# Optimization experiments

Measured on AMD Instinct MI355X. Metric: run time of the kernel, lower is better.

Reference implementation:

```python
import jax, jax.numpy as jnp
import numpy as np

N, E, G = 50000, 800000, 128
F_IN, F0, D, NL, DN = 128, 256, 256, 4, 512


def setup_inputs() -> dict:
    key = jax.random.key(0)
    ks = iter(jax.random.split(key, 40))

    def U(shape, fan_in):
        s = 1.0 / np.sqrt(fan_in)
        return jax.random.uniform(next(ks), shape, minval=-s, maxval=s, dtype=jnp.float32)

    x = jax.random.normal(next(ks), (N, F_IN), dtype=jnp.float32)
    edge_index = jax.random.randint(next(ks), (2, E), 0, N)
    batch_index = jnp.sort(jax.random.randint(next(ks), (N,), 0, G))
    return dict(
        x=x, edge_index=edge_index, batch_index=batch_index,
        fl_W=U((F_IN, F0), F_IN), fl_b=U((F0,), F_IN),
        conv1_W=U((F0, D), F0), conv1_b=U((D,), F0),
        tr1_W=U((D, D), D), tr1_b=U((D,), D),
        bn1_g=jnp.ones((D,), jnp.float32), bn1_b=jnp.zeros((D,), jnp.float32),
        convs_W=U((NL, D, D), D), convs_b=U((NL, D), D),
        trs_W=U((NL, D, D), D), trs_b=U((NL, D), D),
        bns_g=jnp.ones((NL, D), jnp.float32), bns_b=jnp.zeros((NL, D), jnp.float32),
        l1_W=U((2 * D, DN), 2 * D), l1_b=U((DN,), 2 * D),
        l2_W=U((DN, DN // 2), DN), l2_b=U((DN // 2,), DN),
        l3_W=U((DN // 2, 10), DN // 2), l3_b=U((10,), DN // 2),
    )


def reference(x, edge_index, batch_index, fl_W, fl_b, conv1_W, conv1_b,
              tr1_W, tr1_b, bn1_g, bn1_b, convs_W, convs_b, trs_W, trs_b,
              bns_g, bns_b, l1_W, l1_b, l2_W, l2_b, l3_W, l3_b):
    n = x.shape[0]
    loops = jnp.arange(n, dtype=edge_index.dtype)
    src = jnp.concatenate([edge_index[0], loops])  # [E+N] GCN self-loops
    dst = jnp.concatenate([edge_index[1], loops])
    deg = jax.ops.segment_sum(jnp.ones_like(dst, dtype=x.dtype), dst, num_segments=n)
    dis = jax.lax.rsqrt(deg)  # deg >= 1 due to self-loops
    norm = dis[src] * dis[dst]  # [E+N] symmetric normalization

    def gcn(h, W, b):
        m = h @ W
        return jax.ops.segment_sum(norm[:, None] * m[src], dst, num_segments=n) + b

    def bn(h, g, bb):
        mu = h.mean(axis=0)
        var = jnp.mean((h - mu) ** 2, axis=0)  # biased var, torch BN train math
        return g * (h - mu) * jax.lax.rsqrt(var + 1e-5) + bb

    h = x @ fl_W + fl_b
    h = jax.nn.relu(gcn(h, conv1_W, conv1_b))
    h = bn(h, bn1_g, bn1_b)
    h = jax.nn.relu(h @ tr1_W + tr1_b)  # dropout off (eval)
    for i in range(convs_W.shape[0]):
        h = jax.nn.relu(gcn(h, convs_W[i], convs_b[i]))
        h = bn(h, bns_g[i], bns_b[i])
        h = jax.nn.relu(h @ trs_W[i] + trs_b[i])

    sums = jax.ops.segment_sum(h, batch_index, num_segments=G)
    cnt = jax.ops.segment_sum(jnp.ones((n,), h.dtype), batch_index, num_segments=G)
    pooled = sums / jnp.maximum(cnt, 1.0)[:, None]  # global_mean_pool
    z = jnp.concatenate([pooled, pooled], axis=1)
    z = jax.nn.relu(z @ l1_W + l1_b)
    z = jax.nn.relu(z @ l2_W + l2_b)
    return z @ l3_W + l3_b
```

## Files before the change

### kernel.cpp

```cpp
#include <hip/hip_runtime.h>

#define DD 256

typedef unsigned short u16;
typedef unsigned int u32;
using bf16x8 = __attribute__((ext_vector_type(8))) short;
using f16x8  = __attribute__((ext_vector_type(8))) _Float16;
using f32x4  = __attribute__((ext_vector_type(4))) float;

#define GLB_PTR(p) ((const __attribute__((address_space(1))) u32*)(p))
#define LDS_PTR(p) ((__attribute__((address_space(3))) u32*)(p))


__device__ __forceinline__ u32 f2bfx2(float v) {
  u32 b = __float_as_uint(v);
  u32 hi = (b + 0x7fffu + ((b >> 16) & 1u)) >> 16;
  float hf = __uint_as_float(hi << 16);
  float lof = v - hf;
  u32 b2 = __float_as_uint(lof);
  u32 lo = (b2 + 0x7fffu + ((b2 >> 16) & 1u)) >> 16;
  return hi | (lo << 16);
}

__device__ __forceinline__ float bfx2_to_f(u32 e) {
  return __uint_as_float(e << 16) + __uint_as_float(e & 0xffff0000u);
}

__device__ __forceinline__ u16 f2h(float f) {
  _Float16 h = (_Float16)f;
  return __builtin_bit_cast(unsigned short, h);
}
__device__ __forceinline__ float h2f(u16 x) {
  return (float)__builtin_bit_cast(_Float16, x);
}

__device__ __forceinline__ bf16x8 as_bf16x8(uint4 u) {
  union { uint4 u; bf16x8 v; } c;
  c.u = u;
  return c.v;
}
__device__ __forceinline__ f16x8 as_f16x8(uint4 u) {
  union { uint4 u; f16x8 v; } c;
  c.u = u;
  return c.v;
}

__device__ __forceinline__ void unpack8(uint4 a, uint4 b, bf16x8& hi, bf16x8& lo) {
  union { u32 w[4]; bf16x8 v; } H, L;
  H.w[0] = __builtin_amdgcn_perm(a.y, a.x, 0x05040100u);
  L.w[0] = __builtin_amdgcn_perm(a.y, a.x, 0x07060302u);
  H.w[1] = __builtin_amdgcn_perm(a.w, a.z, 0x05040100u);
  L.w[1] = __builtin_amdgcn_perm(a.w, a.z, 0x07060302u);
  H.w[2] = __builtin_amdgcn_perm(b.y, b.x, 0x05040100u);
  L.w[2] = __builtin_amdgcn_perm(b.y, b.x, 0x07060302u);
  H.w[3] = __builtin_amdgcn_perm(b.w, b.z, 0x05040100u);
  L.w[3] = __builtin_amdgcn_perm(b.w, b.z, 0x07060302u);
  hi = H.v;
  lo = L.v;
}

__device__ __forceinline__ int packoff(int col, int k) {
  int w = col >> 6, r = (col >> 4) & 3, c16 = col & 15;
  int kc = k >> 5, q = (k >> 3) & 3, j = k & 7;
  return ((kc * 4 + w) * 4 + r) * 512 + (q * 16 + c16) * 8 + j;
}


__global__ void zero_i32_kernel(int* p, int n) {
  int i = blockIdx.x * 256 + threadIdx.x;
  if (i < n) p[i] = 0;
}

__global__ void zero_f32_kernel(float* p, int n) {
  int i = blockIdx.x * 256 + threadIdx.x;
  if (i < n) p[i] = 0.f;
}

__global__ void count_kernel(const int* __restrict__ dst, int* __restrict__ cnt, int e) {
  int i = blockIdx.x * 256 + threadIdx.x;
  if (i < e) atomicAdd(&cnt[dst[i]], 1);
}

__global__ void scan_block_kernel(const int* __restrict__ cnt, int* __restrict__ out,
                                  int* __restrict__ bsum, int n) {
  __shared__ int sh[256];
  int tid = threadIdx.x;
  int base = blockIdx.x * 1024 + tid * 4;
  int v0 = (base + 0 < n) ? cnt[base + 0] : 0;
  int v1 = (base + 1 < n) ? cnt[base + 1] : 0;
  int v2 = (base + 2 < n) ? cnt[base + 2] : 0;
  int v3 = (base + 3 < n) ? cnt[base + 3] : 0;
  int s = v0 + v1 + v2 + v3;
  sh[tid] = s;
  __syncthreads();
  for (int d = 1; d < 256; d <<= 1) {
    int t = (tid >= d) ? sh[tid - d] : 0;
    __syncthreads();
    sh[tid] += t;
    __syncthreads();
  }
  int excl = sh[tid] - s;
  if (base + 0 < n) out[base + 0] = excl;
  excl += v0;
  if (base + 1 < n) out[base + 1] = excl;
  excl += v1;
  if (base + 2 < n) out[base + 2] = excl;
  excl += v2;
  if (base + 3 < n) out[base + 3] = excl;
  if (tid == 255) bsum[blockIdx.x] = sh[255];
}

__global__ void scan_partials_kernel(int* bsum, int nb) {
  if (threadIdx.x == 0 && blockIdx.x == 0) {
    int acc = 0;
    for (int i = 0; i < nb; ++i) { int t = bsum[i]; bsum[i] = acc; acc += t; }
  }
}

__global__ void finalize_kernel(int* __restrict__ off, const int* __restrict__ bsum,
                                int* __restrict__ cursor, const int* __restrict__ cnt,
                                float* __restrict__ dis, int n, int e) {
  int i = blockIdx.x * 256 + threadIdx.x;
  if (i < n) {
    int o = off[i] + bsum[i >> 10];
    off[i] = o;
    cursor[i] = o;
    dis[i] = rsqrtf((float)(cnt[i] + 1));
  }
  if (i == 0 && blockIdx.x == 0) off[n] = e;
}

__global__ void fill_kernel(const int* __restrict__ src, const int* __restrict__ dst,
                            int* __restrict__ cursor, int* __restrict__ csr_src, int e) {
  int i = blockIdx.x * 256 + threadIdx.x;
  if (i < e) {
    int d = dst[i];
    int p = atomicAdd(&cursor[d], 1);
    csr_src[p] = src[i];
  }
}


__global__ void xsplit_kernel(const float* __restrict__ x, u32* __restrict__ xq, int n) {
  int i = blockIdx.x * 256 + threadIdx.x;
  if (i < n) xq[i] = f2bfx2(x[i]);
}


__global__ void wsplit_all_kernel(const float* __restrict__ fl_W, const float* __restrict__ conv1_W,
                                  const float* __restrict__ convs_W, u16* __restrict__ flHi,
                                  u16* __restrict__ flLo, u16* __restrict__ cvF) {
  int j = blockIdx.x;
  int m = blockIdx.y;
  int k = threadIdx.x;
  if (m == 0) {
    if (k < 128) {
      u32 p = f2bfx2(fl_W[(size_t)k * 256 + j]);
      int off = packoff(j, k);
      flHi[off] = (u16)(p & 0xffffu);
      flLo[off] = (u16)(p >> 16);
    }
  } else {
    int c = m - 1;
    const float* W = (c == 0) ? conv1_W : convs_W + (size_t)(c - 1) * 65536;
    cvF[(size_t)c * 65536 + packoff(j, k)] = f2h(W[(size_t)k * 256 + j]);
  }
}

__global__ void wsplit_fold_kernel(const float* __restrict__ W, const float* __restrict__ scale,
                                   const float* __restrict__ shift, const float* __restrict__ bt,
                                   u16* __restrict__ WhiT, u16* __restrict__ WloT,
                                   float* __restrict__ bias_out) {
  __shared__ float red[256];
  int j = blockIdx.x;
  int k = threadIdx.x;
  float w = W[(size_t)k * 256 + j];
  u32 p = f2bfx2(w * scale[k]);
  int off = packoff(j, k);
  WhiT[off] = (u16)(p & 0xffffu);
  WloT[off] = (u16)(p >> 16);
  red[k] = shift[k] * w;
  __syncthreads();
  for (int d = 128; d > 0; d >>= 1) {
    if (k < d) red[k] += red[k + d];
    __syncthreads();
  }
  if (k == 0) bias_out[j] = bt[j] + red[0];
}


__device__ __forceinline__ void afrag(const u32* Asbase, int R, int q, bf16x8& ah, bf16x8& al) {
  int s = (R & 7) << 4;
  const u32* row = Asbase + R * 32;
  uint4 a0 = *(const uint4*)(row + ((((q * 32)) ^ s) >> 2));
  uint4 a1 = *(const uint4*)(row + ((((q * 32) + 16) ^ s) >> 2));
  unpack8(a0, a1, ah, al);
}

template <int K, bool RELU>
__global__ __launch_bounds__(256) void gemm_mfma_kernel(
    const u32* __restrict__ Aq, const u16* __restrict__ WhiT, const u16* __restrict__ WloT,
    const float* __restrict__ bias, u16* __restrict__ Cv, int nrows) {
  constexpr int NK64 = K / 64;
  __shared__ __align__(16) u32 As[2][4096];
  const int tid = threadIdx.x;
  const int lane = tid & 63;
  const int wave = tid >> 6;
  const int row0 = blockIdx.x * 64;
  const int q = lane >> 4;
  const int r16 = lane & 15;

  int sRowG[4], sOff[4];
#pragma unroll
  for (int c = 0; c < 4; ++c) {
    int row_l = (c & 1) * 32 + wave * 8 + (lane >> 3);
    int grow = row0 + row_l;
    if (grow > nrows - 1) grow = nrows - 1;
    sRowG[c] = grow;
    sOff[c] = ((lane & 7) * 4) ^ ((row_l & 7) << 2);
  }

  int bBase[4];
#pragma unroll
  for (int r = 0; r < 4; ++r) bBase[r] = (wave * 4 + r) * 512 + lane * 8;

  f32x4 acc[4][4];
#pragma unroll
  for (int i = 0; i < 4; ++i)
#pragma unroll
    for (int r = 0; r < 4; ++r) acc[i][r] = (f32x4){0.f, 0.f, 0.f, 0.f};

  auto stage = [&](int buf, int kc64) {
#pragma unroll
    for (int c = 0; c < 4; ++c) {
      int chunk = c >> 1;
      const u32* gsrc = Aq + (size_t)sRowG[c] * K + kc64 * 64 + chunk * 32 + sOff[c];
      u32* ldst = &As[buf][chunk * 2048 + (c & 1) * 1024 + wave * 256];
      __builtin_amdgcn_global_load_lds(GLB_PTR(gsrc), LDS_PTR(ldst), 16, 0, 0);
    }
  };

  stage(0, 0);
  __syncthreads();

  int buf = 0;
#pragma unroll
  for (int kc = 0; kc < NK64; ++kc) {
    if (kc + 1 < NK64) stage(buf ^ 1, kc + 1);
#pragma unroll
    for (int ch = 0; ch < 2; ++ch) {
      const int kc32 = kc * 2 + ch;
      uint4 BH[4], BL[4];
#pragma unroll
      for (int r = 0; r < 4; ++r) {
        BH[r] = *(const uint4*)(WhiT + bBase[r] + kc32 * 8192);
        BL[r] = *(const uint4*)(WloT + bBase[r] + kc32 * 8192);
      }
      bf16x8 ah[4], al[4];
#pragma unroll
      for (int i = 0; i < 4; ++i) afrag(&As[buf][ch * 2048], i * 16 + r16, q, ah[i], al[i]);
#pragma unroll
      for (int r = 0; r < 4; ++r) {
        bf16x8 bh = as_bf16x8(BH[r]);
        bf16x8 bl = as_bf16x8(BL[r]);
#pragma unroll
        for (int i = 0; i < 4; ++i) {
          acc[i][r] = __builtin_amdgcn_mfma_f32_16x16x32_bf16(ah[i], bh, acc[i][r], 0, 0, 0);
          acc[i][r] = __builtin_amdgcn_mfma_f32_16x16x32_bf16(al[i], bh, acc[i][r], 0, 0, 0);
          acc[i][r] = __builtin_amdgcn_mfma_f32_16x16x32_bf16(ah[i], bl, acc[i][r], 0, 0, 0);
        }
      }
    }
    __syncthreads();
    buf ^= 1;
  }

#pragma unroll
  for (int r = 0; r < 4; ++r) {
    int col = wave * 64 + r * 16 + r16;
    float bv = bias ? bias[col] : 0.f;
#pragma unroll
    for (int i = 0; i < 4; ++i) {
#pragma unroll
      for (int g = 0; g < 4; ++g) {
        int row = row0 + i * 16 + q * 4 + g;
        if (row < nrows) {
          float v = acc[i][r][g] + bv;
          if (RELU) v = fmaxf(v, 0.f);
          Cv[(size_t)row * 256 + col] = f2h(v);
        }
      }
    }
  }
}

template <int K1, bool RELU1>
__global__ __launch_bounds__(256) void fused_gemm_kernel(
    const u32* __restrict__ Aq, const u16* __restrict__ W1h, const u16* __restrict__ W1l,
    const float* __restrict__ bias1, const u16* __restrict__ W2f, u16* __restrict__ C,
    int nrows) {
  constexpr int NK1 = K1 / 32;
  __shared__ __align__(16) u32 As[2][2048];
  __shared__ __align__(16) u16 T[64 * 256];
  const int tid = threadIdx.x;
  const int lane = tid & 63;
  const int wave = tid >> 6;
  const int row0 = blockIdx.x * 64;
  const int q = lane >> 4;
  const int r16 = lane & 15;

  int sRowG[2], sOff[2];
#pragma unroll
  for (int c = 0; c < 2; ++c) {
    int row_l = c * 32 + wave * 8 + (lane >> 3);
    int grow = row0 + row_l;
    if (grow > nrows - 1) grow = nrows - 1;
    sRowG[c] = grow;
    sOff[c] = ((lane & 7) * 4) ^ ((row_l & 7) << 2);
  }

  int bBase[4];
#pragma unroll
  for (int r = 0; r < 4; ++r) bBase[r] = (wave * 4 + r) * 512 + lane * 8;

  f32x4 acc[4][4];
#pragma unroll
  for (int i = 0; i < 4; ++i)
#pragma unroll
    for (int r = 0; r < 4; ++r) acc[i][r] = (f32x4){0.f, 0.f, 0.f, 0.f};

  auto stage = [&](int buf, int kc32) {
#pragma unroll
    for (int c = 0; c < 2; ++c) {
      const u32* gsrc = Aq + (size_t)sRowG[c] * K1 + kc32 * 32 + sOff[c];
      u32* ldst = &As[buf][c * 1024 + wave * 256];
      __builtin_amdgcn_global_load_lds(GLB_PTR(gsrc), LDS_PTR(ldst), 16, 0, 0);
    }
  };

  stage(0, 0);
  __syncthreads();
  int buf = 0;
#pragma unroll
  for (int kc = 0; kc < NK1; ++kc) {
    if (kc + 1 < NK1) stage(buf ^ 1, kc + 1);
    uint4 BH[4], BL[4];
#pragma unroll
    for (int r = 0; r < 4; ++r) {
      BH[r] = *(const uint4*)(W1h + bBase[r] + kc * 8192);
      BL[r] = *(const uint4*)(W1l + bBase[r] + kc * 8192);
    }
    bf16x8 ah[4], al[4];
#pragma unroll
    for (int i = 0; i < 4; ++i) afrag(As[buf], i * 16 + r16, q, ah[i], al[i]);
#pragma unroll
    for (int r = 0; r < 4; ++r) {
      bf16x8 bh = as_bf16x8(BH[r]);
      bf16x8 bl = as_bf16x8(BL[r]);
#pragma unroll
      for (int i = 0; i < 4; ++i) {
        acc[i][r] = __builtin_amdgcn_mfma_f32_16x16x32_bf16(ah[i], bh, acc[i][r], 0, 0, 0);
        acc[i][r] = __builtin_amdgcn_mfma_f32_16x16x32_bf16(al[i], bh, acc[i][r], 0, 0, 0);
        acc[i][r] = __builtin_amdgcn_mfma_f32_16x16x32_bf16(ah[i], bl, acc[i][r], 0, 0, 0);
      }
    }
    __syncthreads();
    buf ^= 1;
  }

#pragma unroll
  for (int r = 0; r < 4; ++r) {
    int col = wave * 64 + r * 16 + r16;
    float bv = bias1[col];
#pragma unroll
    for (int i = 0; i < 4; ++i) {
#pragma unroll
      for (int g = 0; g < 4; ++g) {
        int row = i * 16 + q * 4 + g;
        float v = acc[i][r][g] + bv;
        if (RELU1) v = fmaxf(v, 0.f);
        *(u16*)((char*)T + row * 512 + ((col * 2) ^ ((row & 7) << 4))) = f2h(v);
      }
    }
  }

#pragma unroll
  for (int i = 0; i < 4; ++i)
#pragma unroll
    for (int r = 0; r < 4; ++r) acc[i][r] = (f32x4){0.f, 0.f, 0.f, 0.f};

  __syncthreads();

#pragma unroll
  for (int kc = 0; kc < 8; ++kc) {
    uint4 BF[4];
#pragma unroll
    for (int r = 0; r < 4; ++r) BF[r] = *(const uint4*)(W2f + bBase[r] + kc * 8192);
    f16x8 af[4];
#pragma unroll
    for (int i = 0; i < 4; ++i) {
      int row = i * 16 + r16;
      int base = kc * 64 + q * 16;
      af[i] = as_f16x8(*(const uint4*)((char*)T + row * 512 + (base ^ ((row & 7) << 4))));
    }
#pragma unroll
    for (int r = 0; r < 4; ++r) {
      f16x8 bf = as_f16x8(BF[r]);
#pragma unroll
      for (int i = 0; i < 4; ++i)
        acc[i][r] = __builtin_amdgcn_mfma_f32_16x16x32_f16(af[i], bf, acc[i][r], 0, 0, 0);
    }
  }

#pragma unroll
  for (int r = 0; r < 4; ++r) {
    int col = wave * 64 + r * 16 + r16;
#pragma unroll
    for (int i = 0; i < 4; ++i) {
#pragma unroll
      for (int g = 0; g < 4; ++g) {
        int row = row0 + i * 16 + q * 4 + g;
        if (row < nrows) C[(size_t)row * 256 + col] = f2h(acc[i][r][g]);
      }
    }
  }
}


__global__ __launch_bounds__(256) void gather_kernel(
    const u16* __restrict__ m, const int* __restrict__ off,
    const int* __restrict__ csr_src, const float* __restrict__ dis,
    const float* __restrict__ bias, u32* __restrict__ out,
    float* __restrict__ shard, int n) {
  __shared__ float2 red[4][256];
  int wv = threadIdx.x >> 6;
  int lane = threadIdx.x & 63;
  int node = blockIdx.x * 4 + wv;
  float ax = 0.f, ay = 0.f, az = 0.f, aw = 0.f;
  if (node < n) {
    float di = dis[node];
    uint2 v = *(const uint2*)(m + (size_t)node * DD + lane * 4);
    float w = di * di;
    ax = w * h2f((u16)(v.x & 0xffff)); ay = w * h2f((u16)(v.x >> 16));
    az = w * h2f((u16)(v.y & 0xffff)); aw = w * h2f((u16)(v.y >> 16));
    int e0 = off[node], e1 = off[node + 1];
    int e = e0;
    for (; e + 3 < e1; e += 4) {
      int s0 = csr_src[e], s1 = csr_src[e + 1], s2 = csr_src[e + 2], s3 = csr_src[e + 3];
      float w0 = dis[s0] * di, w1 = dis[s1] * di, w2 = dis[s2] * di, w3 = dis[s3] * di;
      uint2 u0 = *(const uint2*)(m + (size_t)s0 * DD + lane * 4);
      uint2 u1 = *(const uint2*)(m + (size_t)s1 * DD + lane * 4);
      uint2 u2 = *(const uint2*)(m + (size_t)s2 * DD + lane * 4);
      uint2 u3 = *(const uint2*)(m + (size_t)s3 * DD + lane * 4);
      ax = fmaf(w0, h2f((u16)(u0.x & 0xffff)), ax); ay = fmaf(w0, h2f((u16)(u0.x >> 16)), ay);
      az = fmaf(w0, h2f((u16)(u0.y & 0xffff)), az); aw = fmaf(w0, h2f((u16)(u0.y >> 16)), aw);
      ax = fmaf(w1, h2f((u16)(u1.x & 0xffff)), ax); ay = fmaf(w1, h2f((u16)(u1.x >> 16)), ay);
      az = fmaf(w1, h2f((u16)(u1.y & 0xffff)), az); aw = fmaf(w1, h2f((u16)(u1.y >> 16)), aw);
      ax = fmaf(w2, h2f((u16)(u2.x & 0xffff)), ax); ay = fmaf(w2, h2f((u16)(u2.x >> 16)), ay);
      az = fmaf(w2, h2f((u16)(u2.y & 0xffff)), az); aw = fmaf(w2, h2f((u16)(u2.y >> 16)), aw);
      ax = fmaf(w3, h2f((u16)(u3.x & 0xffff)), ax); ay = fmaf(w3, h2f((u16)(u3.x >> 16)), ay);
      az = fmaf(w3, h2f((u16)(u3.y & 0xffff)), az); aw = fmaf(w3, h2f((u16)(u3.y >> 16)), aw);
    }
    for (; e < e1; ++e) {
      int s0 = csr_src[e];
      float w0 = dis[s0] * di;
      uint2 u0 = *(const uint2*)(m + (size_t)s0 * DD + lane * 4);
      ax = fmaf(w0, h2f((u16)(u0.x & 0xffff)), ax); ay = fmaf(w0, h2f((u16)(u0.x >> 16)), ay);
      az = fmaf(w0, h2f((u16)(u0.y & 0xffff)), az); aw = fmaf(w0, h2f((u16)(u0.y >> 16)), aw);
    }
    float4 bb = *(const float4*)(bias + lane * 4);
    ax = fmaxf(ax + bb.x, 0.f);
    ay = fmaxf(ay + bb.y, 0.f);
    az = fmaxf(az + bb.z, 0.f);
    aw = fmaxf(aw + bb.w, 0.f);
    uint4 oo;
    oo.x = f2bfx2(ax); oo.y = f2bfx2(ay); oo.z = f2bfx2(az); oo.w = f2bfx2(aw);
    *(uint4*)(out + (size_t)node * DD + lane * 4) = oo;
  }
  red[wv][lane * 4 + 0] = make_float2(ax, ax * ax);
  red[wv][lane * 4 + 1] = make_float2(ay, ay * ay);
  red[wv][lane * 4 + 2] = make_float2(az, az * az);
  red[wv][lane * 4 + 3] = make_float2(aw, aw * aw);
  __syncthreads();
  int c = threadIdx.x;
  float2 a = red[0][c], b2 = red[1][c], c2 = red[2][c], d2 = red[3][c];
  float s = (a.x + b2.x) + (c2.x + d2.x);
  float qq = (a.y + b2.y) + (c2.y + d2.y);
  float* sh = shard + (size_t)(blockIdx.x & 63) * 512;
  atomicAdd(&sh[c], s);
  atomicAdd(&sh[256 + c], qq);
}


__global__ void bn_finalize_kernel(const float* __restrict__ shard, const float* __restrict__ g,
                                   const float* __restrict__ b, float* __restrict__ scale,
                                   float* __restrict__ shift, float inv_n) {
  int c = threadIdx.x;
  float s = 0.f, q = 0.f;
  for (int i = 0; i < 64; ++i) {
    s += shard[(size_t)i * 512 + c];
    q += shard[(size_t)i * 512 + 256 + c];
  }
  float mu = s * inv_n;
  float var = q * inv_n - mu * mu;
  float inv = rsqrtf(var + 1e-5f);
  float sc = g[c] * inv;
  scale[c] = sc;
  shift[c] = b[c] - mu * sc;
}


__global__ void pool_kernel(const u16* __restrict__ h, const int* __restrict__ batch,
                            float* __restrict__ pooled, int n) {
  int g = blockIdx.x;
  int c = threadIdx.x;
  int lo = 0, hi = n;
  while (lo < hi) { int mid = (lo + hi) >> 1; if (batch[mid] < g) lo = mid + 1; else hi = mid; }
  int start = lo;
  hi = n;
  while (lo < hi) { int mid = (lo + hi) >> 1; if (batch[mid] <= g) lo = mid + 1; else hi = mid; }
  int end = lo;
  float a0 = 0.f, a1 = 0.f, a2 = 0.f, a3 = 0.f;
  int r = start;
  for (; r + 3 < end; r += 4) {
    a0 += h2f(h[(size_t)(r + 0) * DD + c]);
    a1 += h2f(h[(size_t)(r + 1) * DD + c]);
    a2 += h2f(h[(size_t)(r + 2) * DD + c]);
    a3 += h2f(h[(size_t)(r + 3) * DD + c]);
  }
  for (; r < end; ++r) a0 += h2f(h[(size_t)r * DD + c]);
  float s = (a0 + a1) + (a2 + a3);
  int cg = end - start;
  pooled[g * DD + c] = s / (float)(cg > 1 ? cg : 1);
}


__global__ void mlp1_kernel(const float* __restrict__ pooled, const float* __restrict__ W,
                            const float* __restrict__ b, float* __restrict__ out) {
  __shared__ float p[256];
  int g = blockIdx.x;
  int j = blockIdx.y * 256 + threadIdx.x;
  p[threadIdx.x] = pooled[g * 256 + threadIdx.x];
  __syncthreads();
  float acc = b[j];
#pragma unroll 8
  for (int k = 0; k < 512; ++k) acc = fmaf(p[k & 255], W[k * 512 + j], acc);
  out[g * 512 + j] = fmaxf(acc, 0.f);
}

__global__ void mlp2_kernel(const float* __restrict__ z1, const float* __restrict__ W,
                            const float* __restrict__ b, float* __restrict__ out) {
  __shared__ float p[512];
  int g = blockIdx.x;
  p[threadIdx.x] = z1[g * 512 + threadIdx.x];
  p[256 + threadIdx.x] = z1[g * 512 + 256 + threadIdx.x];
  __syncthreads();
  float acc = b[threadIdx.x];
#pragma unroll 8
  for (int k = 0; k < 512; ++k) acc = fmaf(p[k], W[k * 256 + threadIdx.x], acc);
  out[g * 256 + threadIdx.x] = fmaxf(acc, 0.f);
}

__global__ void mlp3_kernel(const float* __restrict__ z2, const float* __restrict__ W,
                            const float* __restrict__ b, float* __restrict__ out) {
  int g = blockIdx.x;
  int lane = threadIdx.x;
  float acc[10];
#pragma unroll
  for (int o = 0; o < 10; ++o) acc[o] = 0.f;
  for (int k = lane; k < 256; k += 64) {
    float v = z2[g * 256 + k];
#pragma unroll
    for (int o = 0; o < 10; ++o) acc[o] = fmaf(v, W[k * 10 + o], acc[o]);
  }
#pragma unroll
  for (int o = 0; o < 10; ++o) {
    float s = acc[o];
    for (int d = 32; d > 0; d >>= 1) s += __shfl_down(s, d);
    if (lane == 0) out[g * 10 + o] = s + b[o];
  }
}


extern "C" void kernel_launch(void* const* d_in, const int* in_sizes, int n_in,
                              void* d_out, int out_size, void* d_ws, size_t ws_size,
                              hipStream_t stream) {
  const float* x = (const float*)d_in[0];
  const int* ei = (const int*)d_in[1];
  const int* batch = (const int*)d_in[2];
  const float* fl_W = (const float*)d_in[3];
  const float* fl_b = (const float*)d_in[4];
  const float* conv1_W = (const float*)d_in[5];
  const float* conv1_b = (const float*)d_in[6];
  const float* tr1_W = (const float*)d_in[7];
  const float* tr1_b = (const float*)d_in[8];
  const float* bn1_g = (const float*)d_in[9];
  const float* bn1_b = (const float*)d_in[10];
  const float* convs_W = (const float*)d_in[11];
  const float* convs_b = (const float*)d_in[12];
  const float* trs_W = (const float*)d_in[13];
  const float* trs_b = (const float*)d_in[14];
  const float* bns_g = (const float*)d_in[15];
  const float* bns_b = (const float*)d_in[16];
  const float* l1_W = (const float*)d_in[17];
  const float* l1_b = (const float*)d_in[18];
  const float* l2_W = (const float*)d_in[19];
  const float* l2_b = (const float*)d_in[20];
  const float* l3_W = (const float*)d_in[21];
  const float* l3_b = (const float*)d_in[22];

  const int N = in_sizes[0] / 128;
  const int E = in_sizes[1] / 2;
  const int G = out_size / 10;
  const int NL = in_sizes[11] / (256 * 256);
  const int* src = ei;
  const int* dst = ei + E;

  char* ws = (char*)d_ws;
  size_t o = 0;
  auto alloc = [&](size_t bytes) -> char* {
    o = (o + 255) & ~(size_t)255;
    char* p = ws + o;
    o += bytes;
    return p;
  };
  u32* hA = (u32*)alloc((size_t)N * DD * 4);
  u16* mF = (u16*)alloc((size_t)N * DD * 2);
  u32* xq = (u32*)alloc((size_t)N * 128 * 4);
  float* dis = (float*)alloc((size_t)N * 4);
  int* cnt = (int*)alloc((size_t)N * 4);
  int* off = (int*)alloc((size_t)(N + 1) * 4);
  int* cursor = (int*)alloc((size_t)N * 4);
  int* bsum = (int*)alloc(64 * 4);
  int* csr = (int*)alloc((size_t)E * 4);
  float* shards = (float*)alloc((size_t)(1 + NL) * 64 * 512 * 4);
  float* scalev = (float*)alloc(256 * 4);
  float* shiftv = (float*)alloc(256 * 4);
  float* pooled = (float*)alloc((size_t)G * 256 * 4);
  float* z1 = (float*)alloc((size_t)G * 512 * 4);
  float* z2 = (float*)alloc((size_t)G * 256 * 4);
  u16* flHi = (u16*)alloc(128 * 256 * 2);
  u16* flLo = (u16*)alloc(128 * 256 * 2);
  u16* cvF = (u16*)alloc((size_t)(1 + NL) * 256 * 256 * 2);
  u16* trHi = (u16*)alloc(256 * 256 * 2);
  u16* trLo = (u16*)alloc(256 * 256 * 2);
  float* trBias = (float*)alloc(256 * 4);

  dim3 b256(256);
  const int nblk = (N + 63) / 64;

  zero_i32_kernel<<<(N + 255) / 256, b256, 0, stream>>>(cnt, N);
  count_kernel<<<(E + 255) / 256, b256, 0, stream>>>(dst, cnt, E);
  int nb = (N + 1023) / 1024;
  scan_block_kernel<<<nb, b256, 0, stream>>>(cnt, off, bsum, N);
  scan_partials_kernel<<<1, 64, 0, stream>>>(bsum, nb);
  finalize_kernel<<<(N + 255) / 256, b256, 0, stream>>>(off, bsum, cursor, cnt, dis, N, E);
  fill_kernel<<<(E + 255) / 256, b256, 0, stream>>>(src, dst, cursor, csr, E);

  xsplit_kernel<<<(N * 128 + 255) / 256, b256, 0, stream>>>(x, xq, N * 128);
  dim3 wgrid(256, 2 + NL);
  wsplit_all_kernel<<<wgrid, b256, 0, stream>>>(fl_W, conv1_W, convs_W, flHi, flLo, cvF);
  int shard_elems = (1 + NL) * 64 * 512;
  zero_f32_kernel<<<(shard_elems + 255) / 256, b256, 0, stream>>>(shards, shard_elems);

  fused_gemm_kernel<128, false><<<nblk, b256, 0, stream>>>(xq, flHi, flLo, fl_b, cvF, mF, N);

  for (int L = 0; L < 1 + NL; ++L) {
    const float* bc = (L == 0) ? conv1_b : convs_b + (size_t)(L - 1) * 256;
    const float* gg = (L == 0) ? bn1_g : bns_g + (size_t)(L - 1) * 256;
    const float* gb = (L == 0) ? bn1_b : bns_b + (size_t)(L - 1) * 256;
    const float* Wt = (L == 0) ? tr1_W : trs_W + (size_t)(L - 1) * 256 * 256;
    const float* bt = (L == 0) ? tr1_b : trs_b + (size_t)(L - 1) * 256;
    float* slot = shards + (size_t)L * 64 * 512;

    gather_kernel<<<(N + 3) / 4, b256, 0, stream>>>(mF, off, csr, dis, bc, hA, slot, N);
    bn_finalize_kernel<<<1, b256, 0, stream>>>(slot, gg, gb, scalev, shiftv, 1.0f / (float)N);
    wsplit_fold_kernel<<<256, b256, 0, stream>>>(Wt, scalev, shiftv, bt, trHi, trLo, trBias);
    if (L < NL) {
      fused_gemm_kernel<256, true><<<nblk, b256, 0, stream>>>(
          hA, trHi, trLo, trBias, cvF + (size_t)(L + 1) * 65536, mF, N);
    } else {
      gemm_mfma_kernel<256, true><<<nblk, b256, 0, stream>>>(hA, trHi, trLo, trBias, mF, N);
    }
  }

  pool_kernel<<<G, b256, 0, stream>>>(mF, batch, pooled, N);
  dim3 m1grid(G, 2);
  mlp1_kernel<<<m1grid, b256, 0, stream>>>(pooled, l1_W, l1_b, z1);
  mlp2_kernel<<<G, b256, 0, stream>>>(z1, l2_W, l2_b, z2);
  mlp3_kernel<<<G, 64, 0, stream>>>(z2, l3_W, l3_b, (float*)d_out);
}
```

Measured before the change: 806.3 us.

## Store hidden activations as fp16 and precompute edge weights in CSR

The post-aggregation activations drop from split-bf16 pairs (two values per element) to a single fp16 value. The transform GEMMs therefore run one f16 MFMA per tile instead of three bf16 MFMAs, and read half as many activation bytes. The CSR now stores (src, normalized weight) pairs, so the gather no longer does a dependent dis[src] lookup per edge. In exchange, the BN-folded transform and the activations lose precision, since they are now single fp16 instead of near-fp32 split bf16.

```diff
diff --git a/kernel.cpp b/kernel.cpp
--- a/kernel.cpp
+++ b/kernel.cpp
@@ -20,10 +20,6 @@
   u32 b2 = __float_as_uint(lof);
   u32 lo = (b2 + 0x7fffu + ((b2 >> 16) & 1u)) >> 16;
   return hi | (lo << 16);
-}
-
-__device__ __forceinline__ float bfx2_to_f(u32 e) {
-  return __uint_as_float(e << 16) + __uint_as_float(e & 0xffff0000u);
 }
 
 __device__ __forceinline__ u16 f2h(float f) {
@@ -131,12 +127,15 @@
 }
 
 __global__ void fill_kernel(const int* __restrict__ src, const int* __restrict__ dst,
-                            int* __restrict__ cursor, int* __restrict__ csr_src, int e) {
+                            int* __restrict__ cursor, const float* __restrict__ dis,
+                            int2* __restrict__ csrE, int e) {
   int i = blockIdx.x * 256 + threadIdx.x;
   if (i < e) {
+    int s = src[i];
     int d = dst[i];
     int p = atomicAdd(&cursor[d], 1);
-    csr_src[p] = src[i];
+    float w = dis[s] * dis[d];
+    csrE[p] = make_int2(s, __float_as_int(w));
   }
 }
 
@@ -169,16 +168,12 @@
 
 __global__ void wsplit_fold_kernel(const float* __restrict__ W, const float* __restrict__ scale,
                                    const float* __restrict__ shift, const float* __restrict__ bt,
-                                   u16* __restrict__ WhiT, u16* __restrict__ WloT,
-                                   float* __restrict__ bias_out) {
+                                   u16* __restrict__ trF, float* __restrict__ bias_out) {
   __shared__ float red[256];
   int j = blockIdx.x;
   int k = threadIdx.x;
   float w = W[(size_t)k * 256 + j];
-  u32 p = f2bfx2(w * scale[k]);
-  int off = packoff(j, k);
-  WhiT[off] = (u16)(p & 0xffffu);
-  WloT[off] = (u16)(p >> 16);
+  trF[packoff(j, k)] = f2h(w * scale[k]);
   red[k] = shift[k] * w;
   __syncthreads();
   for (int d = 128; d > 0; d >>= 1) {
@@ -189,7 +184,12 @@
 }
 
 
-__device__ __forceinline__ void afrag(const u32* Asbase, int R, int q, bf16x8& ah, bf16x8& al) {
+__device__ __forceinline__ f16x8 afrag16(const u32* As, int R, int q) {
+  int off = (q * 4) ^ (((R >> 1) & 3) << 2);
+  return as_f16x8(*(const uint4*)(As + R * 16 + off));
+}
+
+__device__ __forceinline__ void afrag32(const u32* Asbase, int R, int q, bf16x8& ah, bf16x8& al) {
   int s = (R & 7) << 4;
   const u32* row = Asbase + R * 32;
   uint4 a0 = *(const uint4*)(row + ((((q * 32)) ^ s) >> 2));
@@ -197,109 +197,11 @@
   unpack8(a0, a1, ah, al);
 }
 
-template <int K, bool RELU>
-__global__ __launch_bounds__(256) void gemm_mfma_kernel(
-    const u32* __restrict__ Aq, const u16* __restrict__ WhiT, const u16* __restrict__ WloT,
-    const float* __restrict__ bias, u16* __restrict__ Cv, int nrows) {
-  constexpr int NK64 = K / 64;
-  __shared__ __align__(16) u32 As[2][4096];
-  const int tid = threadIdx.x;
-  const int lane = tid & 63;
-  const int wave = tid >> 6;
-  const int row0 = blockIdx.x * 64;
-  const int q = lane >> 4;
-  const int r16 = lane & 15;
-
-  int sRowG[4], sOff[4];
-#pragma unroll
-  for (int c = 0; c < 4; ++c) {
-    int row_l = (c & 1) * 32 + wave * 8 + (lane >> 3);
-    int grow = row0 + row_l;
-    if (grow > nrows - 1) grow = nrows - 1;
-    sRowG[c] = grow;
-    sOff[c] = ((lane & 7) * 4) ^ ((row_l & 7) << 2);
-  }
-
-  int bBase[4];
-#pragma unroll
-  for (int r = 0; r < 4; ++r) bBase[r] = (wave * 4 + r) * 512 + lane * 8;
-
-  f32x4 acc[4][4];
-#pragma unroll
-  for (int i = 0; i < 4; ++i)
-#pragma unroll
-    for (int r = 0; r < 4; ++r) acc[i][r] = (f32x4){0.f, 0.f, 0.f, 0.f};
-
-  auto stage = [&](int buf, int kc64) {
-#pragma unroll
-    for (int c = 0; c < 4; ++c) {
-      int chunk = c >> 1;
-      const u32* gsrc = Aq + (size_t)sRowG[c] * K + kc64 * 64 + chunk * 32 + sOff[c];
-      u32* ldst = &As[buf][chunk * 2048 + (c & 1) * 1024 + wave * 256];
-      __builtin_amdgcn_global_load_lds(GLB_PTR(gsrc), LDS_PTR(ldst), 16, 0, 0);
-    }
-  };
-
-  stage(0, 0);
-  __syncthreads();
-
-  int buf = 0;
-#pragma unroll
-  for (int kc = 0; kc < NK64; ++kc) {
-    if (kc + 1 < NK64) stage(buf ^ 1, kc + 1);
-#pragma unroll
-    for (int ch = 0; ch < 2; ++ch) {
-      const int kc32 = kc * 2 + ch;
-      uint4 BH[4], BL[4];
-#pragma unroll
-      for (int r = 0; r < 4; ++r) {
-        BH[r] = *(const uint4*)(WhiT + bBase[r] + kc32 * 8192);
-        BL[r] = *(const uint4*)(WloT + bBase[r] + kc32 * 8192);
-      }
-      bf16x8 ah[4], al[4];
-#pragma unroll
-      for (int i = 0; i < 4; ++i) afrag(&As[buf][ch * 2048], i * 16 + r16, q, ah[i], al[i]);
-#pragma unroll
-      for (int r = 0; r < 4; ++r) {
-        bf16x8 bh = as_bf16x8(BH[r]);
-        bf16x8 bl = as_bf16x8(BL[r]);
-#pragma unroll
-        for (int i = 0; i < 4; ++i) {
-          acc[i][r] = __builtin_amdgcn_mfma_f32_16x16x32_bf16(ah[i], bh, acc[i][r], 0, 0, 0);
-          acc[i][r] = __builtin_amdgcn_mfma_f32_16x16x32_bf16(al[i], bh, acc[i][r], 0, 0, 0);
-          acc[i][r] = __builtin_amdgcn_mfma_f32_16x16x32_bf16(ah[i], bl, acc[i][r], 0, 0, 0);
-        }
-      }
-    }
-    __syncthreads();
-    buf ^= 1;
-  }
-
-#pragma unroll
-  for (int r = 0; r < 4; ++r) {
-    int col = wave * 64 + r * 16 + r16;
-    float bv = bias ? bias[col] : 0.f;
-#pragma unroll
-    for (int i = 0; i < 4; ++i) {
-#pragma unroll
-      for (int g = 0; g < 4; ++g) {
-        int row = row0 + i * 16 + q * 4 + g;
-        if (row < nrows) {
-          float v = acc[i][r][g] + bv;
-          if (RELU) v = fmaxf(v, 0.f);
-          Cv[(size_t)row * 256 + col] = f2h(v);
-        }
-      }
-    }
-  }
-}
-
-template <int K1, bool RELU1>
-__global__ __launch_bounds__(256) void fused_gemm_kernel(
+__global__ __launch_bounds__(256) void fused_fl_kernel(
     const u32* __restrict__ Aq, const u16* __restrict__ W1h, const u16* __restrict__ W1l,
     const float* __restrict__ bias1, const u16* __restrict__ W2f, u16* __restrict__ C,
     int nrows) {
-  constexpr int NK1 = K1 / 32;
+  constexpr int NK1 = 4;
   __shared__ __align__(16) u32 As[2][2048];
   __shared__ __align__(16) u16 T[64 * 256];
   const int tid = threadIdx.x;
@@ -332,7 +234,7 @@
   auto stage = [&](int buf, int kc32) {
 #pragma unroll
     for (int c = 0; c < 2; ++c) {
-      const u32* gsrc = Aq + (size_t)sRowG[c] * K1 + kc32 * 32 + sOff[c];
+      const u32* gsrc = Aq + (size_t)sRowG[c] * 128 + kc32 * 32 + sOff[c];
       u32* ldst = &As[buf][c * 1024 + wave * 256];
       __builtin_amdgcn_global_load_lds(GLB_PTR(gsrc), LDS_PTR(ldst), 16, 0, 0);
     }
@@ -352,7 +254,7 @@
     }
     bf16x8 ah[4], al[4];
 #pragma unroll
-    for (int i = 0; i < 4; ++i) afrag(As[buf], i * 16 + r16, q, ah[i], al[i]);
+    for (int i = 0; i < 4; ++i) afrag32(As[buf], i * 16 + r16, q, ah[i], al[i]);
 #pragma unroll
     for (int r = 0; r < 4; ++r) {
       bf16x8 bh = as_bf16x8(BH[r]);
@@ -378,7 +280,6 @@
       for (int g = 0; g < 4; ++g) {
         int row = i * 16 + q * 4 + g;
         float v = acc[i][r][g] + bv;
-        if (RELU1) v = fmaxf(v, 0.f);
         *(u16*)((char*)T + row * 512 + ((col * 2) ^ ((row & 7) << 4))) = f2h(v);
       }
     }
@@ -388,7 +289,6 @@
   for (int i = 0; i < 4; ++i)
 #pragma unroll
     for (int r = 0; r < 4; ++r) acc[i][r] = (f32x4){0.f, 0.f, 0.f, 0.f};
-
   __syncthreads();
 
 #pragma unroll
@@ -426,11 +326,193 @@
   }
 }
 
+__global__ __launch_bounds__(256) void fused_h_kernel(
+    const u16* __restrict__ Ah, const u16* __restrict__ W1f, const float* __restrict__ bias1,
+    const u16* __restrict__ W2f, u16* __restrict__ C, int nrows) {
+  __shared__ __align__(16) u32 As[2][1024];
+  __shared__ __align__(16) u16 T[64 * 256];
+  const int tid = threadIdx.x;
+  const int lane = tid & 63;
+  const int wave = tid >> 6;
+  const int row0 = blockIdx.x * 64;
+  const int q = lane >> 4;
+  const int r16 = lane & 15;
+
+  int row_l = tid >> 2;
+  int grow = row0 + row_l;
+  if (grow > nrows - 1) grow = nrows - 1;
+  const int sK = (((tid & 3) * 8)) ^ (((row_l >> 1) & 3) << 3);
+
+  int bBase[4];
+#pragma unroll
+  for (int r = 0; r < 4; ++r) bBase[r] = (wave * 4 + r) * 512 + lane * 8;
+
+  f32x4 acc[4][4];
+#pragma unroll
+  for (int i = 0; i < 4; ++i)
+#pragma unroll
+    for (int r = 0; r < 4; ++r) acc[i][r] = (f32x4){0.f, 0.f, 0.f, 0.f};
+
+  auto stage = [&](int buf, int kc32) {
+    const u16* gsrc = Ah + (size_t)grow * 256 + kc32 * 32 + sK;
+    u32* ldst = &As[buf][wave * 256];
+    __builtin_amdgcn_global_load_lds(GLB_PTR(gsrc), LDS_PTR(ldst), 16, 0, 0);
+  };
+
+  stage(0, 0);
+  __syncthreads();
+  int buf = 0;
+#pragma unroll
+  for (int kc = 0; kc < 8; ++kc) {
+    if (kc + 1 < 8) stage(buf ^ 1, kc + 1);
+    uint4 BF[4];
+#pragma unroll
+    for (int r = 0; r < 4; ++r) BF[r] = *(const uint4*)(W1f + bBase[r] + kc * 8192);
+    f16x8 af[4];
+#pragma unroll
+    for (int i = 0; i < 4; ++i) af[i] = afrag16(As[buf], i * 16 + r16, q);
+#pragma unroll
+    for (int r = 0; r < 4; ++r) {
+      f16x8 bf = as_f16x8(BF[r]);
+#pragma unroll
+      for (int i = 0; i < 4; ++i)
+        acc[i][r] = __builtin_amdgcn_mfma_f32_16x16x32_f16(af[i], bf, acc[i][r], 0, 0, 0);
+    }
+    __syncthreads();
+    buf ^= 1;
+  }
+
+#pragma unroll
+  for (int r = 0; r < 4; ++r) {
+    int col = wave * 64 + r * 16 + r16;
+    float bv = bias1[col];
+#pragma unroll
+    for (int i = 0; i < 4; ++i) {
+#pragma unroll
+      for (int g = 0; g < 4; ++g) {
+        int row = i * 16 + q * 4 + g;
+        float v = fmaxf(acc[i][r][g] + bv, 0.f);
+        *(u16*)((char*)T + row * 512 + ((col * 2) ^ ((row & 7) << 4))) = f2h(v);
+      }
+    }
+  }
+
+#pragma unroll
+  for (int i = 0; i < 4; ++i)
+#pragma unroll
+    for (int r = 0; r < 4; ++r) acc[i][r] = (f32x4){0.f, 0.f, 0.f, 0.f};
+  __syncthreads();
+
+#pragma unroll
+  for (int kc = 0; kc < 8; ++kc) {
+    uint4 BF[4];
+#pragma unroll
+    for (int r = 0; r < 4; ++r) BF[r] = *(const uint4*)(W2f + bBase[r] + kc * 8192);
+    f16x8 af[4];
+#pragma unroll
+    for (int i = 0; i < 4; ++i) {
+      int row = i * 16 + r16;
+      int base = kc * 64 + q * 16;
+      af[i] = as_f16x8(*(const uint4*)((char*)T + row * 512 + (base ^ ((row & 7) << 4))));
+    }
+#pragma unroll
+    for (int r = 0; r < 4; ++r) {
+      f16x8 bf = as_f16x8(BF[r]);
+#pragma unroll
+      for (int i = 0; i < 4; ++i)
+        acc[i][r] = __builtin_amdgcn_mfma_f32_16x16x32_f16(af[i], bf, acc[i][r], 0, 0, 0);
+    }
+  }
+
+#pragma unroll
+  for (int r = 0; r < 4; ++r) {
+    int col = wave * 64 + r * 16 + r16;
+#pragma unroll
+    for (int i = 0; i < 4; ++i) {
+#pragma unroll
+      for (int g = 0; g < 4; ++g) {
+        int row = row0 + i * 16 + q * 4 + g;
+        if (row < nrows) C[(size_t)row * 256 + col] = f2h(acc[i][r][g]);
+      }
+    }
+  }
+}
+
+__global__ __launch_bounds__(256) void gemm_h_kernel(
+    const u16* __restrict__ Ah, const u16* __restrict__ W1f, const float* __restrict__ bias,
+    u16* __restrict__ C, int nrows) {
+  __shared__ __align__(16) u32 As[2][1024];
+  const int tid = threadIdx.x;
+  const int lane = tid & 63;
+  const int wave = tid >> 6;
+  const int row0 = blockIdx.x * 64;
+  const int q = lane >> 4;
+  const int r16 = lane & 15;
+
+  int row_l = tid >> 2;
+  int grow = row0 + row_l;
+  if (grow > nrows - 1) grow = nrows - 1;
+  const int sK = (((tid & 3) * 8)) ^ (((row_l >> 1) & 3) << 3);
+
+  int bBase[4];
+#pragma unroll
+  for (int r = 0; r < 4; ++r) bBase[r] = (wave * 4 + r) * 512 + lane * 8;
+
+  f32x4 acc[4][4];
+#pragma unroll
+  for (int i = 0; i < 4; ++i)
+#pragma unroll
+    for (int r = 0; r < 4; ++r) acc[i][r] = (f32x4){0.f, 0.f, 0.f, 0.f};
+
+  auto stage = [&](int buf, int kc32) {
+    const u16* gsrc = Ah + (size_t)grow * 256 + kc32 * 32 + sK;
+    u32* ldst = &As[buf][wave * 256];
+    __builtin_amdgcn_global_load_lds(GLB_PTR(gsrc), LDS_PTR(ldst), 16, 0, 0);
+  };
+
+  stage(0, 0);
+  __syncthreads();
+  int buf = 0;
+#pragma unroll
+  for (int kc = 0; kc < 8; ++kc) {
+    if (kc + 1 < 8) stage(buf ^ 1, kc + 1);
+    uint4 BF[4];
+#pragma unroll
+    for (int r = 0; r < 4; ++r) BF[r] = *(const uint4*)(W1f + bBase[r] + kc * 8192);
+    f16x8 af[4];
+#pragma unroll
+    for (int i = 0; i < 4; ++i) af[i] = afrag16(As[buf], i * 16 + r16, q);
+#pragma unroll
+    for (int r = 0; r < 4; ++r) {
+      f16x8 bf = as_f16x8(BF[r]);
+#pragma unroll
+      for (int i = 0; i < 4; ++i)
+        acc[i][r] = __builtin_amdgcn_mfma_f32_16x16x32_f16(af[i], bf, acc[i][r], 0, 0, 0);
+    }
+    __syncthreads();
+    buf ^= 1;
+  }
+
+#pragma unroll
+  for (int r = 0; r < 4; ++r) {
+    int col = wave * 64 + r * 16 + r16;
+    float bv = bias[col];
+#pragma unroll
+    for (int i = 0; i < 4; ++i) {
+#pragma unroll
+      for (int g = 0; g < 4; ++g) {
+        int row = row0 + i * 16 + q * 4 + g;
+        if (row < nrows) C[(size_t)row * 256 + col] = f2h(fmaxf(acc[i][r][g] + bv, 0.f));
+      }
+    }
+  }
+}
+
 
 __global__ __launch_bounds__(256) void gather_kernel(
     const u16* __restrict__ m, const int* __restrict__ off,
-    const int* __restrict__ csr_src, const float* __restrict__ dis,
-    const float* __restrict__ bias, u32* __restrict__ out,
+    const int2* __restrict__ csrE, const float* __restrict__ dis,
+    const float* __restrict__ bias, u16* __restrict__ out,
     float* __restrict__ shard, int n) {
   __shared__ float2 red[4][256];
   int wv = threadIdx.x >> 6;
@@ -446,12 +528,13 @@
     int e0 = off[node], e1 = off[node + 1];
     int e = e0;
     for (; e + 3 < e1; e += 4) {
-      int s0 = csr_src[e], s1 = csr_src[e + 1], s2 = csr_src[e + 2], s3 = csr_src[e + 3];
-      float w0 = dis[s0] * di, w1 = dis[s1] * di, w2 = dis[s2] * di, w3 = dis[s3] * di;
-      uint2 u0 = *(const uint2*)(m + (size_t)s0 * DD + lane * 4);
-      uint2 u1 = *(const uint2*)(m + (size_t)s1 * DD + lane * 4);
-      uint2 u2 = *(const uint2*)(m + (size_t)s2 * DD + lane * 4);
-      uint2 u3 = *(const uint2*)(m + (size_t)s3 * DD + lane * 4);
+      int2 p0 = csrE[e], p1 = csrE[e + 1], p2 = csrE[e + 2], p3 = csrE[e + 3];
+      float w0 = __int_as_float(p0.y), w1 = __int_as_float(p1.y);
+      float w2 = __int_as_float(p2.y), w3 = __int_as_float(p3.y);
+      uint2 u0 = *(const uint2*)(m + (size_t)p0.x * DD + lane * 4);
+      uint2 u1 = *(const uint2*)(m + (size_t)p1.x * DD + lane * 4);
+      uint2 u2 = *(const uint2*)(m + (size_t)p2.x * DD + lane * 4);
+      uint2 u3 = *(const uint2*)(m + (size_t)p3.x * DD + lane * 4);
       ax = fmaf(w0, h2f((u16)(u0.x & 0xffff)), ax); ay = fmaf(w0, h2f((u16)(u0.x >> 16)), ay);
       az = fmaf(w0, h2f((u16)(u0.y & 0xffff)), az); aw = fmaf(w0, h2f((u16)(u0.y >> 16)), aw);
       ax = fmaf(w1, h2f((u16)(u1.x & 0xffff)), ax); ay = fmaf(w1, h2f((u16)(u1.x >> 16)), ay);
@@ -462,9 +545,9 @@
       az = fmaf(w3, h2f((u16)(u3.y & 0xffff)), az); aw = fmaf(w3, h2f((u16)(u3.y >> 16)), aw);
     }
     for (; e < e1; ++e) {
-      int s0 = csr_src[e];
-      float w0 = dis[s0] * di;
-      uint2 u0 = *(const uint2*)(m + (size_t)s0 * DD + lane * 4);
+      int2 p0 = csrE[e];
+      float w0 = __int_as_float(p0.y);
+      uint2 u0 = *(const uint2*)(m + (size_t)p0.x * DD + lane * 4);
       ax = fmaf(w0, h2f((u16)(u0.x & 0xffff)), ax); ay = fmaf(w0, h2f((u16)(u0.x >> 16)), ay);
       az = fmaf(w0, h2f((u16)(u0.y & 0xffff)), az); aw = fmaf(w0, h2f((u16)(u0.y >> 16)), aw);
     }
@@ -473,9 +556,10 @@
     ay = fmaxf(ay + bb.y, 0.f);
     az = fmaxf(az + bb.z, 0.f);
     aw = fmaxf(aw + bb.w, 0.f);
-    uint4 oo;
-    oo.x = f2bfx2(ax); oo.y = f2bfx2(ay); oo.z = f2bfx2(az); oo.w = f2bfx2(aw);
-    *(uint4*)(out + (size_t)node * DD + lane * 4) = oo;
+    uint2 oo;
+    oo.x = (u32)f2h(ax) | ((u32)f2h(ay) << 16);
+    oo.y = (u32)f2h(az) | ((u32)f2h(aw) << 16);
+    *(uint2*)(out + (size_t)node * DD + lane * 4) = oo;
   }
   red[wv][lane * 4 + 0] = make_float2(ax, ax * ax);
   red[wv][lane * 4 + 1] = make_float2(ay, ay * ay);
@@ -624,7 +708,7 @@
     o += bytes;
     return p;
   };
-  u32* hA = (u32*)alloc((size_t)N * DD * 4);
+  u16* hA = (u16*)alloc((size_t)N * DD * 2);
   u16* mF = (u16*)alloc((size_t)N * DD * 2);
   u32* xq = (u32*)alloc((size_t)N * 128 * 4);
   float* dis = (float*)alloc((size_t)N * 4);
@@ -632,7 +716,7 @@
   int* off = (int*)alloc((size_t)(N + 1) * 4);
   int* cursor = (int*)alloc((size_t)N * 4);
   int* bsum = (int*)alloc(64 * 4);
-  int* csr = (int*)alloc((size_t)E * 4);
+  int2* csrE = (int2*)alloc((size_t)E * 8);
   float* shards = (float*)alloc((size_t)(1 + NL) * 64 * 512 * 4);
   float* scalev = (float*)alloc(256 * 4);
   float* shiftv = (float*)alloc(256 * 4);
@@ -642,8 +726,7 @@
   u16* flHi = (u16*)alloc(128 * 256 * 2);
   u16* flLo = (u16*)alloc(128 * 256 * 2);
   u16* cvF = (u16*)alloc((size_t)(1 + NL) * 256 * 256 * 2);
-  u16* trHi = (u16*)alloc(256 * 256 * 2);
-  u16* trLo = (u16*)alloc(256 * 256 * 2);
+  u16* trF = (u16*)alloc(256 * 256 * 2);
   float* trBias = (float*)alloc(256 * 4);
 
   dim3 b256(256);
@@ -655,7 +738,7 @@
   scan_block_kernel<<<nb, b256, 0, stream>>>(cnt, off, bsum, N);
   scan_partials_kernel<<<1, 64, 0, stream>>>(bsum, nb);
   finalize_kernel<<<(N + 255) / 256, b256, 0, stream>>>(off, bsum, cursor, cnt, dis, N, E);
-  fill_kernel<<<(E + 255) / 256, b256, 0, stream>>>(src, dst, cursor, csr, E);
+  fill_kernel<<<(E + 255) / 256, b256, 0, stream>>>(src, dst, cursor, dis, csrE, E);
 
   xsplit_kernel<<<(N * 128 + 255) / 256, b256, 0, stream>>>(x, xq, N * 128);
   dim3 wgrid(256, 2 + NL);
@@ -663,7 +746,7 @@
   int shard_elems = (1 + NL) * 64 * 512;
   zero_f32_kernel<<<(shard_elems + 255) / 256, b256, 0, stream>>>(shards, shard_elems);
 
-  fused_gemm_kernel<128, false><<<nblk, b256, 0, stream>>>(xq, flHi, flLo, fl_b, cvF, mF, N);
+  fused_fl_kernel<<<nblk, b256, 0, stream>>>(xq, flHi, flLo, fl_b, cvF, mF, N);
 
   for (int L = 0; L < 1 + NL; ++L) {
     const float* bc = (L == 0) ? conv1_b : convs_b + (size_t)(L - 1) * 256;
@@ -673,14 +756,14 @@
     const float* bt = (L == 0) ? tr1_b : trs_b + (size_t)(L - 1) * 256;
     float* slot = shards + (size_t)L * 64 * 512;
 
-    gather_kernel<<<(N + 3) / 4, b256, 0, stream>>>(mF, off, csr, dis, bc, hA, slot, N);
+    gather_kernel<<<(N + 3) / 4, b256, 0, stream>>>(mF, off, csrE, dis, bc, hA, slot, N);
     bn_finalize_kernel<<<1, b256, 0, stream>>>(slot, gg, gb, scalev, shiftv, 1.0f / (float)N);
-    wsplit_fold_kernel<<<256, b256, 0, stream>>>(Wt, scalev, shiftv, bt, trHi, trLo, trBias);
+    wsplit_fold_kernel<<<256, b256, 0, stream>>>(Wt, scalev, shiftv, bt, trF, trBias);
     if (L < NL) {
-      fused_gemm_kernel<256, true><<<nblk, b256, 0, stream>>>(
-          hA, trHi, trLo, trBias, cvF + (size_t)(L + 1) * 65536, mF, N);
+      fused_h_kernel<<<nblk, b256, 0, stream>>>(hA, trF, trBias,
+                                                cvF + (size_t)(L + 1) * 65536, mF, N);
     } else {
-      gemm_mfma_kernel<256, true><<<nblk, b256, 0, stream>>>(hA, trHi, trLo, trBias, mF, N);
+      gemm_h_kernel<<<nblk, b256, 0, stream>>>(hA, trF, trBias, mF, N);
     }
   }
 
```

New measurement: 750.5 us. 1.07x faster.
